# Optimization experiments

Hardware: AMD Instinct MI355X
Metric: run time of the kernel (lower is better)

## Reference

```python
import jax, jax.numpy as jnp
import numpy as np

D_MODEL = 1024
N_HEAD = 16
HEAD_DIM = D_MODEL // N_HEAD
B, S = 4, 2048


def setup_inputs() -> dict:
    key = jax.random.key(0)
    ks = jax.random.split(key, 11)
    scale = 1.0 / np.sqrt(D_MODEL)
    inp = {
        "q": jax.random.normal(ks[0], (B, S, D_MODEL), jnp.float32),
        "k": jax.random.normal(ks[1], (B, S, D_MODEL), jnp.float32),
        "v": jax.random.normal(ks[2], (B, S, D_MODEL), jnp.float32),
        # torch nn.Linear weights: [out_features, in_features], y = x @ W.T + b
        "Wq": jax.random.normal(ks[3], (D_MODEL, D_MODEL), jnp.float32) * scale,
        "bq": jax.random.normal(ks[4], (D_MODEL,), jnp.float32) * scale,
        "Wk": jax.random.normal(ks[5], (D_MODEL, D_MODEL), jnp.float32) * scale,
        "bk": jax.random.normal(ks[6], (D_MODEL,), jnp.float32) * scale,
        "Wv": jax.random.normal(ks[7], (D_MODEL, D_MODEL), jnp.float32) * scale,
        "bv": jax.random.normal(ks[8], (D_MODEL,), jnp.float32) * scale,
        "Wo": jax.random.normal(ks[9], (D_MODEL, D_MODEL), jnp.float32) * scale,
        "bo": jax.random.normal(ks[10], (D_MODEL,), jnp.float32) * scale,
    }
    return inp


def _split_heads(x):
    # [B, S, D] -> [B, H, S, hd]
    b, s, _ = x.shape
    return x.reshape(b, s, N_HEAD, HEAD_DIM).transpose(0, 2, 1, 3)


def reference(q, k, v, Wq, bq, Wk, bk, Wv, bv, Wo, bo):
    qh = _split_heads(q @ Wq.T + bq)
    kh = _split_heads(k @ Wk.T + bk)
    vh = _split_heads(v @ Wv.T + bv)
    scores = jnp.einsum("bhqd,bhkd->bhqk", qh, kh) / jnp.sqrt(
        jnp.asarray(HEAD_DIM, qh.dtype)
    )
    weights = jax.nn.softmax(scores, axis=-1)  # [B, H, Sq, Sk]
    ctx = jnp.einsum("bhqk,bhkd->bhqd", weights, vh)
    b, h, s, d = ctx.shape
    ctx = ctx.transpose(0, 2, 1, 3).reshape(b, s, h * d)  # [B, S, D]
    return ctx @ Wo.T + bo
```

## Files before the change

kernel.cpp:

```cpp
#include <hip/hip_runtime.h>
#include <hip/hip_bf16.h>

typedef float   f32x4   __attribute__((ext_vector_type(4)));
typedef __bf16  bf16x8  __attribute__((ext_vector_type(8)));
typedef unsigned short u16x8 __attribute__((ext_vector_type(8)));
typedef unsigned short u16x4 __attribute__((ext_vector_type(4)));

#define DEVI __device__ __forceinline__

DEVI unsigned short f2bf_bits(float f) {
    __bf16 h = (__bf16)f;
    return __builtin_bit_cast(unsigned short, h);
}

DEVI f32x4 mfma_bf16(bf16x8 a, bf16x8 b, f32x4 c) {
    return __builtin_amdgcn_mfma_f32_16x16x32_bf16(a, b, c, 0, 0, 0);
}

DEVI float fast_exp2(float x) {
#if __has_builtin(__builtin_amdgcn_exp2f)
    return __builtin_amdgcn_exp2f(x);
#else
    float r;
    asm("v_exp_f32 %0, %1" : "=v"(r) : "v"(x));
    return r;
#endif
}

template <bool A_F32, bool OUT_F32>
__global__ __launch_bounds__(256) void gemm_bt_kernel(
    const void* __restrict__ Ap, const float* __restrict__ W,
    const float* __restrict__ bias, void* __restrict__ Cp,
    int M, int N, int K, float scale)
{
    __shared__ __align__(16) char ldsA[128 * 128];
    __shared__ __align__(16) char ldsB[128 * 128];
    const int t = threadIdx.x;
    const int wave = t >> 6, lane = t & 63;
    const int g = lane >> 4, c = lane & 15;
    const int rowbase = blockIdx.x * 128;
    const int colbase = blockIdx.y * 128;
    const int wr = (wave >> 1) * 64, wc = (wave & 1) * 64;

    f32x4 acc[4][4] = {};

    for (int kt = 0; kt < K; kt += 64) {
#pragma unroll
        for (int ch = 0; ch < 4; ++ch) {
            int id = ch * 256 + t;
            int row = id >> 3;
            int col = (id & 7) * 8;
            int dst = row * 128 + ((col * 2) ^ ((row & 7) << 4));
            u16x8 hv;
            if constexpr (A_F32) {
                const float* src = (const float*)Ap + (size_t)(rowbase + row) * K + kt + col;
                f32x4 x0 = *(const f32x4*)src;
                f32x4 x1 = *(const f32x4*)(src + 4);
#pragma unroll
                for (int j = 0; j < 4; ++j) { hv[j] = f2bf_bits(x0[j]); hv[4 + j] = f2bf_bits(x1[j]); }
            } else {
                const unsigned short* src = (const unsigned short*)Ap + (size_t)(rowbase + row) * K + kt + col;
                hv = *(const u16x8*)src;
            }
            *(u16x8*)(ldsA + dst) = hv;

            const float* srcb = W + (size_t)(colbase + row) * K + kt + col;
            f32x4 y0 = *(const f32x4*)srcb;
            f32x4 y1 = *(const f32x4*)(srcb + 4);
            u16x8 hb;
#pragma unroll
            for (int j = 0; j < 4; ++j) { hb[j] = f2bf_bits(y0[j]); hb[4 + j] = f2bf_bits(y1[j]); }
            *(u16x8*)(ldsB + dst) = hb;
        }
        __syncthreads();

#pragma unroll
        for (int kk = 0; kk < 2; ++kk) {
            bf16x8 af[4], bfr[4];
#pragma unroll
            for (int i = 0; i < 4; ++i) {
                int ra = wr + i * 16 + c;
                af[i] = *(const bf16x8*)(ldsA + ra * 128 + ((kk * 64 + g * 16) ^ ((ra & 7) << 4)));
                int rb = wc + i * 16 + c;
                bfr[i] = *(const bf16x8*)(ldsB + rb * 128 + ((kk * 64 + g * 16) ^ ((rb & 7) << 4)));
            }
#pragma unroll
            for (int i = 0; i < 4; ++i)
#pragma unroll
                for (int j = 0; j < 4; ++j)
                    acc[i][j] = mfma_bf16(af[i], bfr[j], acc[i][j]);
        }
        __syncthreads();
    }

#pragma unroll
    for (int j = 0; j < 4; ++j) {
        int coln = colbase + wc + j * 16 + c;
        float bv = bias[coln];
#pragma unroll
        for (int i = 0; i < 4; ++i) {
            int row0 = rowbase + wr + i * 16 + g * 4;
#pragma unroll
            for (int r = 0; r < 4; ++r) {
                float val = (acc[i][j][r] + bv) * scale;
                if constexpr (OUT_F32)
                    ((float*)Cp)[(size_t)(row0 + r) * N + coln] = val;
                else
                    ((unsigned short*)Cp)[(size_t)(row0 + r) * N + coln] = f2bf_bits(val);
            }
        }
    }
}

__global__ __launch_bounds__(256) void transpose_v_kernel(
    const unsigned short* __restrict__ Vp, unsigned short* __restrict__ Vt)
{
    __shared__ unsigned short tile[64][72];
    const int t = threadIdx.x;
    const int bh = blockIdx.y, b = bh >> 4, h = bh & 15;
    const int s0 = blockIdx.x * 64;
#pragma unroll
    for (int ch = 0; ch < 2; ++ch) {
        int id = ch * 256 + t;
        int srow = id >> 3, dcol = (id & 7) * 8;
        u16x8 v = *(const u16x8*)(Vp + (size_t)(b * 2048 + s0 + srow) * 1024 + h * 64 + dcol);
        *(u16x8*)&tile[srow][dcol] = v;
    }
    __syncthreads();
#pragma unroll
    for (int ch = 0; ch < 2; ++ch) {
        int id = ch * 256 + t;
        int drow = id >> 3, scol = (id & 7) * 8;
        u16x8 ov;
#pragma unroll
        for (int j = 0; j < 8; ++j) ov[j] = tile[scol + j][drow];
        *(u16x8*)(Vt + (size_t)(bh * 64 + drow) * 2048 + s0 + scol) = ov;
    }
}

__global__ __launch_bounds__(256) void attn_kernel(
    const unsigned short* __restrict__ Qp, const unsigned short* __restrict__ Kp,
    const unsigned short* __restrict__ Vt, unsigned short* __restrict__ ctx)
{
    __shared__ __align__(16) char ldsK[64 * 128];
    __shared__ __align__(16) char ldsV[64 * 128];
    __shared__ __align__(16) char ldsP[4][2][16 * 128];
    const int t = threadIdx.x;
    const int wave = t >> 6, lane = t & 63;
    const int g = lane >> 4, c = lane & 15;
    const int bh = blockIdx.y, b = bh >> 4, h = bh & 15;
    const int qb = blockIdx.x * 128;

    bf16x8 qf0[2], qf1[2];
    {
        const unsigned short* q0 = Qp + (size_t)(b * 2048 + qb + wave * 32 + c) * 1024 + h * 64;
        qf0[0] = *(const bf16x8*)(q0 + 8 * g);
        qf0[1] = *(const bf16x8*)(q0 + 32 + 8 * g);
        const unsigned short* q1 = q0 + (size_t)16 * 1024;
        qf1[0] = *(const bf16x8*)(q1 + 8 * g);
        qf1[1] = *(const bf16x8*)(q1 + 32 + 8 * g);
    }

    f32x4 o0[4] = {}, o1[4] = {};
    float psum0 = 0.f, psum1 = 0.f;

    const int row0 = t >> 3, colB = (t & 7) * 8;
    const int row1 = 32 + row0;
    const int dst0 = row0 * 128 + ((colB * 2) ^ ((row0 & 7) << 4));
    const int dst1 = row1 * 128 + ((colB * 2) ^ ((row1 & 7) << 4));
    const unsigned short* Ksrc = Kp + (size_t)(b * 2048) * 1024 + h * 64;
    const unsigned short* Vsrc = Vt + (size_t)(bh * 64) * 2048;

    u16x8 kv0 = *(const u16x8*)(Ksrc + (size_t)row0 * 1024 + colB);
    u16x8 kv1 = *(const u16x8*)(Ksrc + (size_t)row1 * 1024 + colB);
    u16x8 vv0 = *(const u16x8*)(Vsrc + (size_t)row0 * 2048 + colB);
    u16x8 vv1 = *(const u16x8*)(Vsrc + (size_t)row1 * 2048 + colB);

    char* pw0 = ldsP[wave][0];
    char* pw1 = ldsP[wave][1];

    for (int kb = 0; kb < 2048; kb += 64) {
        *(u16x8*)(ldsK + dst0) = kv0;
        *(u16x8*)(ldsK + dst1) = kv1;
        *(u16x8*)(ldsV + dst0) = vv0;
        *(u16x8*)(ldsV + dst1) = vv1;
        __syncthreads();

        if (kb + 64 < 2048) {
            kv0 = *(const u16x8*)(Ksrc + (size_t)(kb + 64 + row0) * 1024 + colB);
            kv1 = *(const u16x8*)(Ksrc + (size_t)(kb + 64 + row1) * 1024 + colB);
            vv0 = *(const u16x8*)(Vsrc + (size_t)row0 * 2048 + kb + 64 + colB);
            vv1 = *(const u16x8*)(Vsrc + (size_t)row1 * 2048 + kb + 64 + colB);
        }

        f32x4 s0[4] = {}, s1[4] = {};
#pragma unroll
        for (int kk = 0; kk < 2; ++kk) {
            bf16x8 kf[4];
#pragma unroll
            for (int ti = 0; ti < 4; ++ti) {
                int rk = ti * 16 + c;
                kf[ti] = *(const bf16x8*)(ldsK + rk * 128 + ((kk * 64 + g * 16) ^ ((rk & 7) << 4)));
            }
#pragma unroll
            for (int ti = 0; ti < 4; ++ti) {
                s0[ti] = mfma_bf16(kf[ti], qf0[kk], s0[ti]);
                s1[ti] = mfma_bf16(kf[ti], qf1[kk], s1[ti]);
            }
        }

#pragma unroll
        for (int ti = 0; ti < 4; ++ti) {
            float p0 = fast_exp2(s0[ti][0]);
            float p1 = fast_exp2(s0[ti][1]);
            float p2 = fast_exp2(s0[ti][2]);
            float p3 = fast_exp2(s0[ti][3]);
            psum0 += (p0 + p1) + (p2 + p3);
            u16x4 hp;
            hp[0] = f2bf_bits(p0); hp[1] = f2bf_bits(p1);
            hp[2] = f2bf_bits(p2); hp[3] = f2bf_bits(p3);
            *(u16x4*)(pw0 + c * 128 + ((ti * 32 + g * 8) ^ ((c & 7) << 4))) = hp;
        }
#pragma unroll
        for (int ti = 0; ti < 4; ++ti) {
            float p0 = fast_exp2(s1[ti][0]);
            float p1 = fast_exp2(s1[ti][1]);
            float p2 = fast_exp2(s1[ti][2]);
            float p3 = fast_exp2(s1[ti][3]);
            psum1 += (p0 + p1) + (p2 + p3);
            u16x4 hp;
            hp[0] = f2bf_bits(p0); hp[1] = f2bf_bits(p1);
            hp[2] = f2bf_bits(p2); hp[3] = f2bf_bits(p3);
            *(u16x4*)(pw1 + c * 128 + ((ti * 32 + g * 8) ^ ((c & 7) << 4))) = hp;
        }

#pragma unroll
        for (int kk = 0; kk < 2; ++kk) {
            bf16x8 vf[4];
#pragma unroll
            for (int ti = 0; ti < 4; ++ti) {
                int rv = ti * 16 + c;
                vf[ti] = *(const bf16x8*)(ldsV + rv * 128 + ((kk * 64 + g * 16) ^ ((rv & 7) << 4)));
            }
            bf16x8 pa0 = *(const bf16x8*)(pw0 + c * 128 + ((kk * 64 + g * 16) ^ ((c & 7) << 4)));
            bf16x8 pa1 = *(const bf16x8*)(pw1 + c * 128 + ((kk * 64 + g * 16) ^ ((c & 7) << 4)));
#pragma unroll
            for (int ti = 0; ti < 4; ++ti) {
                o0[ti] = mfma_bf16(pa0, vf[ti], o0[ti]);
                o1[ti] = mfma_bf16(pa1, vf[ti], o1[ti]);
            }
        }
        __syncthreads();
    }

    psum0 += __shfl_xor(psum0, 16);
    psum0 += __shfl_xor(psum0, 32);
    psum1 += __shfl_xor(psum1, 16);
    psum1 += __shfl_xor(psum1, 32);

#pragma unroll
    for (int r = 0; r < 4; ++r) {
        float inv0 = 1.0f / __shfl(psum0, 4 * g + r);
        float inv1 = 1.0f / __shfl(psum1, 4 * g + r);
        int row0q = qb + wave * 32 + 4 * g + r;
        int row1q = row0q + 16;
#pragma unroll
        for (int ti = 0; ti < 4; ++ti) {
            int col = h * 64 + ti * 16 + c;
            ctx[(size_t)(b * 2048 + row0q) * 1024 + col] = f2bf_bits(o0[ti][r] * inv0);
            ctx[(size_t)(b * 2048 + row1q) * 1024 + col] = f2bf_bits(o1[ti][r] * inv1);
        }
    }
}

extern "C" void kernel_launch(void* const* d_in, const int* in_sizes, int n_in,
                              void* d_out, int out_size, void* d_ws, size_t ws_size,
                              hipStream_t stream)
{
    const float* q  = (const float*)d_in[0];
    const float* k  = (const float*)d_in[1];
    const float* v  = (const float*)d_in[2];
    const float* Wq = (const float*)d_in[3];
    const float* bq = (const float*)d_in[4];
    const float* Wk = (const float*)d_in[5];
    const float* bk = (const float*)d_in[6];
    const float* Wv = (const float*)d_in[7];
    const float* bv = (const float*)d_in[8];
    const float* Wo = (const float*)d_in[9];
    const float* bo = (const float*)d_in[10];
    float* out = (float*)d_out;

    char* ws = (char*)d_ws;
    const size_t SZ = (size_t)8192 * 1024 * 2;
    unsigned short* Qp = (unsigned short*)(ws);
    unsigned short* Kp = (unsigned short*)(ws + SZ);
    unsigned short* Vp = (unsigned short*)(ws + 2 * SZ);
    unsigned short* Vt = (unsigned short*)(ws + 3 * SZ);
    unsigned short* ctx = Vp;

    const float QSCALE = 0.1803368801111244f;

    dim3 gg(64, 8);
    gemm_bt_kernel<true, false><<<gg, 256, 0, stream>>>(q, Wq, bq, Qp, 8192, 1024, 1024, QSCALE);
    gemm_bt_kernel<true, false><<<gg, 256, 0, stream>>>(k, Wk, bk, Kp, 8192, 1024, 1024, 1.0f);
    gemm_bt_kernel<true, false><<<gg, 256, 0, stream>>>(v, Wv, bv, Vp, 8192, 1024, 1024, 1.0f);
    transpose_v_kernel<<<dim3(32, 64), 256, 0, stream>>>(Vp, Vt);
    attn_kernel<<<dim3(16, 64), 256, 0, stream>>>(Qp, Kp, Vt, ctx);
    gemm_bt_kernel<false, true><<<dim3(64, 8), 256, 0, stream>>>(ctx, Wo, bo, out, 8192, 1024, 1024, 1.0f);
}
```

Before: 235.8 us.

## Pre-convert QKV weights to bf16 and load bf16 tiles via async global-to-LDS

A new kernel converts Wq/Wk/Wv to bf16 once per call into the Vt workspace slot, which is free until the transpose runs. The projection GEMMs then load the bf16 weight tile straight into LDS with global_load_lds, and the output GEMM does the same for the bf16 ctx operand. The other operand is still converted from fp32 through registers. This halves weight read traffic and removes conversion work inside the GEMM loop, at the cost of an extra launch and one write of the bf16 weights. The async loads use an XOR slot swizzle that must match the existing LDS read pattern.

```diff
diff --git a/kernel.cpp b/kernel.cpp
--- a/kernel.cpp
+++ b/kernel.cpp
@@ -27,9 +27,31 @@
 #endif
 }
 
-template <bool A_F32, bool OUT_F32>
+DEVI void gload16(const void* g, void* l) {
+    __builtin_amdgcn_global_load_lds(
+        (const __attribute__((address_space(1))) void*)g,
+        (__attribute__((address_space(3))) void*)l, 16, 0, 0);
+}
+
+__global__ __launch_bounds__(256) void convert_w_kernel(
+    const float* __restrict__ Wq, const float* __restrict__ Wk,
+    const float* __restrict__ Wv, unsigned short* __restrict__ Wb)
+{
+    int idx = blockIdx.x * 256 + threadIdx.x;
+    int which = idx >> 17;
+    int off = (idx & 131071) * 8;
+    const float* src = which == 0 ? Wq : (which == 1 ? Wk : Wv);
+    f32x4 a = *(const f32x4*)(src + off);
+    f32x4 b = *(const f32x4*)(src + off + 4);
+    u16x8 h;
+#pragma unroll
+    for (int j = 0; j < 4; ++j) { h[j] = f2bf_bits(a[j]); h[4 + j] = f2bf_bits(b[j]); }
+    *(u16x8*)(Wb + (size_t)which * 1048576 + off) = h;
+}
+
+template <bool A_ASYNC, bool OUT_F32>
 __global__ __launch_bounds__(256) void gemm_bt_kernel(
-    const void* __restrict__ Ap, const float* __restrict__ W,
+    const void* __restrict__ Ap, const void* __restrict__ Wp,
     const float* __restrict__ bias, void* __restrict__ Cp,
     int M, int N, int K, float scale)
 {
@@ -42,35 +64,52 @@
     const int colbase = blockIdx.y * 128;
     const int wr = (wave >> 1) * 64, wc = (wave & 1) * 64;
 
+    const int arow = lane >> 3;
+    const int aslot = (lane & 7) ^ arow;
+
     f32x4 acc[4][4] = {};
 
     for (int kt = 0; kt < K; kt += 64) {
+        if constexpr (A_ASYNC) {
+            const unsigned short* Ab = (const unsigned short*)Ap;
+#pragma unroll
+            for (int j = 0; j < 4; ++j) {
+                int rg = wave * 4 + j;
+                int row = rg * 8 + arow;
+                gload16(Ab + (size_t)(rowbase + row) * K + kt + aslot * 8,
+                        ldsA + rg * 1024);
+            }
+        } else {
+            const unsigned short* Wb = (const unsigned short*)Wp;
+#pragma unroll
+            for (int j = 0; j < 4; ++j) {
+                int rg = wave * 4 + j;
+                int row = rg * 8 + arow;
+                gload16(Wb + (size_t)(colbase + row) * K + kt + aslot * 8,
+                        ldsB + rg * 1024);
+            }
+        }
+
 #pragma unroll
         for (int ch = 0; ch < 4; ++ch) {
             int id = ch * 256 + t;
             int row = id >> 3;
             int col = (id & 7) * 8;
             int dst = row * 128 + ((col * 2) ^ ((row & 7) << 4));
+            const float* src;
+            if constexpr (A_ASYNC)
+                src = (const float*)Wp + (size_t)(colbase + row) * K + kt + col;
+            else
+                src = (const float*)Ap + (size_t)(rowbase + row) * K + kt + col;
+            f32x4 x0 = *(const f32x4*)src;
+            f32x4 x1 = *(const f32x4*)(src + 4);
             u16x8 hv;
-            if constexpr (A_F32) {
-                const float* src = (const float*)Ap + (size_t)(rowbase + row) * K + kt + col;
-                f32x4 x0 = *(const f32x4*)src;
-                f32x4 x1 = *(const f32x4*)(src + 4);
-#pragma unroll
-                for (int j = 0; j < 4; ++j) { hv[j] = f2bf_bits(x0[j]); hv[4 + j] = f2bf_bits(x1[j]); }
-            } else {
-                const unsigned short* src = (const unsigned short*)Ap + (size_t)(rowbase + row) * K + kt + col;
-                hv = *(const u16x8*)src;
-            }
-            *(u16x8*)(ldsA + dst) = hv;
-
-            const float* srcb = W + (size_t)(colbase + row) * K + kt + col;
-            f32x4 y0 = *(const f32x4*)srcb;
-            f32x4 y1 = *(const f32x4*)(srcb + 4);
-            u16x8 hb;
-#pragma unroll
-            for (int j = 0; j < 4; ++j) { hb[j] = f2bf_bits(y0[j]); hb[4 + j] = f2bf_bits(y1[j]); }
-            *(u16x8*)(ldsB + dst) = hb;
+#pragma unroll
+            for (int j = 0; j < 4; ++j) { hv[j] = f2bf_bits(x0[j]); hv[4 + j] = f2bf_bits(x1[j]); }
+            if constexpr (A_ASYNC)
+                *(u16x8*)(ldsB + dst) = hv;
+            else
+                *(u16x8*)(ldsA + dst) = hv;
         }
         __syncthreads();
 
@@ -297,14 +336,17 @@
     unsigned short* Vp = (unsigned short*)(ws + 2 * SZ);
     unsigned short* Vt = (unsigned short*)(ws + 3 * SZ);
     unsigned short* ctx = Vp;
+    unsigned short* Wbf = Vt;
 
     const float QSCALE = 0.1803368801111244f;
 
+    convert_w_kernel<<<dim3(1536), 256, 0, stream>>>(Wq, Wk, Wv, Wbf);
+
     dim3 gg(64, 8);
-    gemm_bt_kernel<true, false><<<gg, 256, 0, stream>>>(q, Wq, bq, Qp, 8192, 1024, 1024, QSCALE);
-    gemm_bt_kernel<true, false><<<gg, 256, 0, stream>>>(k, Wk, bk, Kp, 8192, 1024, 1024, 1.0f);
-    gemm_bt_kernel<true, false><<<gg, 256, 0, stream>>>(v, Wv, bv, Vp, 8192, 1024, 1024, 1.0f);
+    gemm_bt_kernel<false, false><<<gg, 256, 0, stream>>>(q, Wbf,           bq, Qp, 8192, 1024, 1024, QSCALE);
+    gemm_bt_kernel<false, false><<<gg, 256, 0, stream>>>(k, Wbf + 1048576, bk, Kp, 8192, 1024, 1024, 1.0f);
+    gemm_bt_kernel<false, false><<<gg, 256, 0, stream>>>(v, Wbf + 2097152, bv, Vp, 8192, 1024, 1024, 1.0f);
     transpose_v_kernel<<<dim3(32, 64), 256, 0, stream>>>(Vp, Vt);
     attn_kernel<<<dim3(16, 64), 256, 0, stream>>>(Qp, Kp, Vt, ctx);
-    gemm_bt_kernel<false, true><<<dim3(64, 8), 256, 0, stream>>>(ctx, Wo, bo, out, 8192, 1024, 1024, 1.0f);
-}
+    gemm_bt_kernel<true, true><<<gg, 256, 0, stream>>>(ctx, Wo, bo, out, 8192, 1024, 1024, 1.0f);
+}
```

Measured after the change: 227.3 us. -3.6%, faster.
